# Kernel optimization log

Measured on AMD Instinct MI355X. Metric: run time of the kernel, lower is better.

## Reference

```python
import jax, jax.numpy as jnp
import numpy as np
from jax import lax

B, S, D_MODEL, H, D_CONV, CHUNK = 8, 4096, 1024, 16, 4, 64
D_INNER = D_MODEL


def setup_inputs() -> dict:
    key = jax.random.key(0)
    ks = jax.random.split(key, 6)
    x = jax.random.normal(ks[0], (B, S, D_MODEL), jnp.float32)
    in_proj_w = jax.random.normal(ks[1], (D_INNER + H, D_MODEL), jnp.float32) * 0.02
    conv_w = jax.random.normal(ks[2], (D_INNER, 1, D_CONV), jnp.float32) * 0.3
    conv_b = jnp.zeros((D_INNER,), jnp.float32)
    w_base = jax.random.uniform(ks[3], (H,), jnp.float32, minval=-0.5, maxval=0.5)
    out_proj_w = jax.random.normal(ks[4], (D_MODEL, D_INNER), jnp.float32) * 0.02
    return {"x": x, "in_proj_w": in_proj_w, "conv_w": conv_w, "conv_b": conv_b,
            "w_base": w_base, "out_proj_w": out_proj_w}


def _segsum(a):
    # a: (..., T) -> (..., T, T) with out[i, j] = sum_{k=j+1..i} a[k] for i>=j else -inf
    T = a.shape[-1]
    lower_strict = jnp.tril(jnp.ones((T, T), bool), -1)   # row i > col j
    lower = jnp.tril(jnp.ones((T, T), bool), 0)
    xr = jnp.where(lower_strict, a[..., :, None], 0.0)    # (..., T, T)
    s = jnp.cumsum(xr, axis=-2)
    return jnp.where(lower, s, -jnp.inf)


def _ssd(x, A, l):
    # x: (b, s, h, n); A: (b, s, h); l = chunk size
    b, s, h, n = x.shape
    c = s // l
    x = x.reshape(b, c, l, h, n)
    A = A.reshape(b, c, l, h).transpose(0, 3, 1, 2)        # (b, h, c, l)
    A_cumsum = jnp.cumsum(A, axis=-1)

    # intra-chunk (diagonal) part
    L_log = _segsum(A)                                      # (b, h, c, l, l)
    L = jnp.exp(L_log - jnp.max(L_log, axis=-1, keepdims=True))
    norm_diag = L.sum(-1).transpose(0, 2, 3, 1)             # (b, c, l, h)
    Y_diag = jnp.einsum('bhcls,bcshn->bclhn', L, x)

    # chunk states
    decay_states = A_cumsum[..., -1:] - A_cumsum            # (b, h, c, l)
    decay_states = jnp.exp(decay_states - jnp.max(decay_states, axis=-1, keepdims=True))
    norm_decay = decay_states.sum(-1).transpose(0, 2, 1)    # (b, c, h)
    states = jnp.einsum('bhcl,bclhn->bchn', decay_states, x)

    norm_decay = jnp.pad(norm_decay, ((0, 0), (1, 0), (0, 0)))
    states = jnp.pad(states, ((0, 0), (1, 0), (0, 0), (0, 0)))

    # inter-chunk recurrence
    decay_chunk = _segsum(jnp.pad(A_cumsum[..., -1], ((0, 0), (0, 0), (1, 0))))  # (b,h,c+1,c+1)
    decay_chunk = jnp.exp(decay_chunk - jnp.max(decay_chunk, axis=-1, keepdims=True))
    norm_decay = jnp.einsum('bhzc,bch->bzh', decay_chunk, norm_decay)[:, :-1]    # (b, c, h)
    states = jnp.einsum('bhzc,bchn->bzhn', decay_chunk, states)[:, :-1]          # (b, c, h, n)

    # off-diagonal output
    state_decay_out = jnp.exp(A_cumsum - jnp.max(A_cumsum, axis=-1, keepdims=True))
    norm_off = jnp.einsum('bch,bhcl->bclh', norm_decay, state_decay_out)
    Y_off = jnp.einsum('bchn,bhcl->bclhn', states, state_decay_out)

    Y = (Y_diag + Y_off).reshape(b, s, h, n)
    norm = (norm_diag + norm_off).reshape(b, s, h)
    return Y / norm[..., None]


def reference(x, in_proj_w, conv_w, conv_b, w_base, out_proj_w):
    b, s, d_model = x.shape
    d_inner = in_proj_w.shape[0] - H
    xw = jnp.einsum('bsd,ed->bse', x, in_proj_w)            # (b, s, d_inner + H)
    xi, w = xw[..., :d_inner], xw[..., d_inner:]            # (b,s,d_inner), (b,s,H)
    # causal depthwise conv (padding k-1 on the left == pad both + slice [:s])
    xc = lax.conv_general_dilated(
        xi.transpose(0, 2, 1), conv_w, window_strides=(1,),
        padding=[(D_CONV - 1, 0)], feature_group_count=d_inner,
        dimension_numbers=('NCH', 'OIH', 'NCH'))
    xc = (xc + conv_b[None, :, None]).transpose(0, 2, 1)    # (b, s, d_inner)
    xh = xc.reshape(b, s, H, d_inner // H)                  # (b, s, h, n)
    A = w * w_base                                          # (b, s, H)
    y = _ssd(xh, A, CHUNK)                                  # (b, s, h, n)
    y = y.reshape(b, s, d_inner)
    return jnp.einsum('bsd,ed->bse', y, out_proj_w)         # (b, s, d_model)
```

## Files before the change

### kernel.cpp

```cpp
#include <hip/hip_runtime.h>
#include <hip/hip_bf16.h>
#include <cstdint>

#define B_ 8
#define S_ 4096
#define DM 1024
#define H_ 16
#define DN 64
#define CH 64
#define NC 64
#define M_ (B_ * S_)

typedef unsigned short u16;
typedef u16 u16x8 __attribute__((ext_vector_type(8)));
typedef u16 u16x4 __attribute__((ext_vector_type(4)));
typedef float f32x4 __attribute__((ext_vector_type(4)));
typedef __bf16 bf16x8 __attribute__((ext_vector_type(8)));

__device__ __forceinline__ float bf2f(u16 u) { return __uint_as_float(((unsigned)u) << 16); }
__device__ __forceinline__ u16 f2bf(float f) { __bf16 h = (__bf16)f; return __builtin_bit_cast(u16, h); }

#define GLOAD16(gp, lp) \
  __builtin_amdgcn_global_load_lds((__attribute__((address_space(1))) const void*)(gp), \
                                   (__attribute__((address_space(3))) void*)(lp), 16, 0, 0)
#define BAR()   asm volatile("s_barrier" ::: "memory")
#define VMCNT4() asm volatile("s_waitcnt vmcnt(4)" ::: "memory")
#define VMCNT0() asm volatile("s_waitcnt vmcnt(0)" ::: "memory")

__device__ __forceinline__ void stage_unit(const u16* __restrict__ src, int row0, int kt,
                                           int ks, u16* ldsu, int t, int K) {
#pragma unroll
  for (int i = 0; i < 2; ++i) {
    int f = i * 512 + t;
    int row = f >> 2, j = f & 3;
    int g = j ^ ((row >> 1) & 3);
    GLOAD16(src + (size_t)(row0 + row) * K + kt * 64 + ks * 32 + g * 8, ldsu + f * 8);
  }
}

__device__ __forceinline__ void lda4(bf16x8* fr, const u16* unit, int rbase, int lr, int lk) {
#pragma unroll
  for (int q = 0; q < 4; ++q) {
    int row = rbase + q * 16 + lr;
    int cell = row * 4 + (lk ^ ((row >> 1) & 3));
    fr[q] = *reinterpret_cast<const bf16x8*>(&unit[cell * 8]);
  }
}

__device__ __forceinline__ void mfma16(f32x4 (&acc)[8][4], int mh, const bf16x8* aF, const bf16x8* bF) {
  __builtin_amdgcn_s_setprio(1);
#pragma unroll
  for (int q = 0; q < 4; ++q)
#pragma unroll
    for (int nf = 0; nf < 4; ++nf)
      acc[mh * 4 + q][nf] = __builtin_amdgcn_mfma_f32_16x16x32_bf16(aF[q], bF[nf], acc[mh * 4 + q][nf], 0, 0, 0);
  __builtin_amdgcn_s_setprio(0);
}

template<int MODE>
__global__ __launch_bounds__(512, 2) void bgemm8(
    const u16* __restrict__ A, const u16* __restrict__ Bw,
    void* __restrict__ Cout, int K)
{
  __shared__ u16 lds[8][8192];
  const int orig = blockIdx.x;
  const int swz  = (orig & 7) * 64 + (orig >> 3);
  const int m0 = (swz >> 2) * 256;
  const int n0 = (swz & 3) * 256;
  const int t  = threadIdx.x;
  const int wid = t >> 6, l = t & 63;
  const int wm = wid >> 2, wn = wid & 3;
  const int lr = l & 15, lk = l >> 4;
  const int arb = wm * 128;
  const int brb = wn * 64;

  f32x4 acc[8][4];
#pragma unroll
  for (int i = 0; i < 8; ++i)
#pragma unroll
    for (int j = 0; j < 4; ++j) acc[i][j] = (f32x4){0.f, 0.f, 0.f, 0.f};

  stage_unit(A,  m0, 0, 0, lds[0], t, K);
  stage_unit(Bw, n0, 0, 0, lds[2], t, K);
  stage_unit(A,  m0, 0, 1, lds[1], t, K);
  stage_unit(Bw, n0, 0, 1, lds[3], t, K);
  stage_unit(Bw, n0, 1, 0, lds[6], t, K);
  stage_unit(Bw, n0, 1, 1, lds[7], t, K);
  VMCNT4();
  BAR();

  bf16x8 aF[4], bF0[4], bF1[4];
  for (int i = 0; i < 8; ++i) {
    const bool st = (i < 7);
    lda4(aF, lds[0], arb, lr, lk);
    lda4(bF0, lds[2], brb, lr, lk);
    stage_unit(A, m0, 2 * i + 1, 0, lds[4], t, K);
    BAR(); mfma16(acc, 0, aF, bF0);
    lda4(aF, lds[1], arb, lr, lk);
    lda4(bF1, lds[3], brb, lr, lk);
    stage_unit(A, m0, 2 * i + 1, 1, lds[5], t, K);
    BAR(); mfma16(acc, 0, aF, bF1);
    lda4(aF, lds[0], arb + 64, lr, lk);
    if (st) stage_unit(Bw, n0, 2 * i + 2, 0, lds[2], t, K);
    BAR(); mfma16(acc, 1, aF, bF0);
    lda4(aF, lds[1], arb + 64, lr, lk);
    if (st) stage_unit(Bw, n0, 2 * i + 2, 1, lds[3], t, K);
    if (st) VMCNT4(); else VMCNT0();
    BAR(); mfma16(acc, 1, aF, bF1);
    lda4(aF, lds[4], arb, lr, lk);
    lda4(bF0, lds[6], brb, lr, lk);
    if (st) stage_unit(A, m0, 2 * i + 2, 0, lds[0], t, K);
    BAR(); mfma16(acc, 0, aF, bF0);
    lda4(aF, lds[5], arb, lr, lk);
    lda4(bF1, lds[7], brb, lr, lk);
    if (st) stage_unit(A, m0, 2 * i + 2, 1, lds[1], t, K);
    BAR(); mfma16(acc, 0, aF, bF1);
    lda4(aF, lds[4], arb + 64, lr, lk);
    if (st) stage_unit(Bw, n0, 2 * i + 3, 0, lds[6], t, K);
    BAR(); mfma16(acc, 1, aF, bF0);
    lda4(aF, lds[5], arb + 64, lr, lk);
    if (st) stage_unit(Bw, n0, 2 * i + 3, 1, lds[7], t, K);
    if (st) VMCNT4();
    BAR(); mfma16(acc, 1, aF, bF1);
  }

#pragma unroll
  for (int mf = 0; mf < 8; ++mf) {
#pragma unroll
    for (int nf = 0; nf < 4; ++nf) {
      int n  = n0 + wn * 64 + nf * 16 + lr;
      int mb = m0 + wm * 128 + mf * 16 + lk * 4;
#pragma unroll
      for (int r = 0; r < 4; ++r) {
        if (MODE == 0) ((float*)Cout)[(size_t)(mb + r) * 1024 + n] = acc[mf][nf][r];
        else           ((u16*)Cout)[(size_t)(mb + r) * 1024 + n] = f2bf(acc[mf][nf][r]);
      }
    }
  }
}

__global__ __launch_bounds__(256) void prep_kernel(
    const float* __restrict__ ipw, const float* __restrict__ opw,
    u16* __restrict__ wbf_in, u16* __restrict__ wbf_out, u16* __restrict__ wlo)
{
  int b = blockIdx.x;
  if (b < 1032) {
    const float* src = (b < 520) ? ipw : opw;
    u16* dst = (b < 520) ? wbf_in : wbf_out;
    size_t i = ((size_t)(b < 520 ? b : b - 520) * 256 + threadIdx.x) * 8;
    f32x4 a = *reinterpret_cast<const f32x4*>(&src[i]);
    f32x4 c = *reinterpret_cast<const f32x4*>(&src[i + 4]);
    u16x8 o;
#pragma unroll
    for (int j = 0; j < 4; ++j) { o[j] = f2bf(a[j]); o[4 + j] = f2bf(c[j]); }
    *reinterpret_cast<u16x8*>(&dst[i]) = o;
  } else {
    size_t e = ((size_t)(b - 1032) * 256 + threadIdx.x) * 8;
    f32x4 a = *reinterpret_cast<const f32x4*>(&ipw[1048576 + e]);
    f32x4 c = *reinterpret_cast<const f32x4*>(&ipw[1048576 + e + 4]);
    u16x8 o;
#pragma unroll
    for (int j = 0; j < 4; ++j) {
      u16 h = f2bf(a[j]); o[j]     = f2bf(a[j] - bf2f(h));
      u16 g = f2bf(c[j]); o[4 + j] = f2bf(c[j] - bf2f(g));
    }
    *reinterpret_cast<u16x8*>(&wlo[e]) = o;
  }
}

__global__ __launch_bounds__(256) void wsplit(
    const float* __restrict__ x, const u16* __restrict__ wbf, const u16* __restrict__ wlo,
    u16* __restrict__ xbf, float* __restrict__ wbufT)
{
  __shared__ u16 hi[4][16 * 5 * 8];
  __shared__ u16 lo[4][16 * 5 * 8];
  __shared__ float comb[3][64][4];
  const int t = threadIdx.x;
  const int w = t >> 6, l = t & 63;
  const int r0 = blockIdx.x * 16;
  const int k0 = w * 256;
  const int lr = l & 15, lk = l >> 4;
  const int srow = l >> 2, skc = l & 3;
  u16* HI = hi[w];
  u16* LO = lo[w];

  const float* gx  = &x[(size_t)(r0 + srow) * 1024 + k0 + skc * 8];
  const u16*   gbh = &wbf[(size_t)(1024 + lr) * 1024 + k0 + lk * 8];
  const u16*   gbl = &wlo[(size_t)lr * 1024 + k0 + lk * 8];

  f32x4 a0 = *reinterpret_cast<const f32x4*>(gx);
  f32x4 a1 = *reinterpret_cast<const f32x4*>(gx + 4);
  bf16x8 bh = *reinterpret_cast<const bf16x8*>(gbh);
  bf16x8 bl = *reinterpret_cast<const bf16x8*>(gbl);

  f32x4 acc = (f32x4){0.f, 0.f, 0.f, 0.f};
  const int wcell = srow * 5 + skc;
  const int rcell = lr * 5 + lk;

  for (int kt = 0; kt < 8; ++kt) {
    f32x4 n0, n1; bf16x8 nbh, nbl;
    if (kt < 7) {
      n0  = *reinterpret_cast<const f32x4*>(gx + (kt + 1) * 32);
      n1  = *reinterpret_cast<const f32x4*>(gx + (kt + 1) * 32 + 4);
      nbh = *reinterpret_cast<const bf16x8*>(gbh + (kt + 1) * 32);
      nbl = *reinterpret_cast<const bf16x8*>(gbl + (kt + 1) * 32);
    }
    u16x8 h8, l8;
#pragma unroll
    for (int j = 0; j < 4; ++j) {
      u16 ha = f2bf(a0[j]); h8[j]     = ha; l8[j]     = f2bf(a0[j] - bf2f(ha));
      u16 hb = f2bf(a1[j]); h8[4 + j] = hb; l8[4 + j] = f2bf(a1[j] - bf2f(hb));
    }
    *reinterpret_cast<u16x8*>(&xbf[(size_t)(r0 + srow) * 1024 + k0 + kt * 32 + skc * 8]) = h8;
    *reinterpret_cast<u16x8*>(&HI[wcell * 8]) = h8;
    *reinterpret_cast<u16x8*>(&LO[wcell * 8]) = l8;
    asm volatile("s_waitcnt lgkmcnt(0)" ::: "memory");
    __builtin_amdgcn_sched_barrier(0);
    bf16x8 ah = *reinterpret_cast<const bf16x8*>(&HI[rcell * 8]);
    bf16x8 al = *reinterpret_cast<const bf16x8*>(&LO[rcell * 8]);
    acc = __builtin_amdgcn_mfma_f32_16x16x32_bf16(ah, bh, acc, 0, 0, 0);
    acc = __builtin_amdgcn_mfma_f32_16x16x32_bf16(al, bh, acc, 0, 0, 0);
    acc = __builtin_amdgcn_mfma_f32_16x16x32_bf16(ah, bl, acc, 0, 0, 0);
    a0 = n0; a1 = n1; bh = nbh; bl = nbl;
  }
  if (w) {
#pragma unroll
    for (int r = 0; r < 4; ++r) comb[w - 1][l][r] = acc[r];
  }
  __syncthreads();
  if (!w) {
#pragma unroll
    for (int r = 0; r < 4; ++r) acc[r] += comb[0][l][r] + comb[1][l][r] + comb[2][l][r];
    *reinterpret_cast<f32x4*>(&wbufT[(size_t)lr * M_ + r0 + lk * 4]) = acc;
  }
}

__global__ __launch_bounds__(256) void statesk(
    const u16* __restrict__ xi, const float* __restrict__ cw, const float* __restrict__ cb,
    const float* __restrict__ wbufT, const float* __restrict__ w_base,
    float* __restrict__ Acum, float* __restrict__ acbuf,
    float* __restrict__ states, float* __restrict__ ndbuf)
{
  int bi = blockIdx.x;
  int c  = bi & 63;
  int h  = (bi >> 6) & 15;
  int b  = bi >> 10;
  int bh = b * 16 + h;
  int t  = threadIdx.x;
  __shared__ u16 xis[67][64];
  __shared__ u16 xsT[64][66];
  __shared__ float dsv[CH];
  __shared__ float wls[4][64];
  __shared__ float cbs[64];
  size_t m0 = (size_t)b * S_ + (size_t)c * CH;
  size_t abase = ((size_t)bh * NC + c) * CH;

  wls[t & 3][t >> 2] = cw[(size_t)h * 256 + t];
  if (t < 64) cbs[t] = cb[h * 64 + t];

  {
    int g8  = t & 7;
    int hr0 = t >> 3;
    for (int hr = hr0; hr < 67; hr += 32) {
      u16x8 v = {0, 0, 0, 0, 0, 0, 0, 0};
      if (!(c == 0 && hr < 3))
        v = *reinterpret_cast<const u16x8*>(&xi[(m0 - 3 + hr) * DM + h * 64 + g8 * 8]);
      *reinterpret_cast<u16x8*>(&xis[hr][g8 * 8]) = v;
    }
  }

  if (t < 64) {
    float p = wbufT[(size_t)h * M_ + m0 + t] * w_base[h];
#pragma unroll
    for (int off = 1; off < 64; off <<= 1) {
      float v = __shfl_up(p, off);
      if (t >= off) p += v;
    }
    Acum[abase + t] = p;
    if (t == 63) acbuf[(size_t)bh * NC + c] = p;
    float rmin = p;
#pragma unroll
    for (int off = 1; off < 64; off <<= 1) {
      float v = __shfl_up(rmin, off);
      if (t >= off) rmin = fminf(rmin, v);
    }
    float minall = __shfl(rmin, 63);
    dsv[t] = __expf(minall - p);
  }
  __syncthreads();

  {
    int n  = t & 63;
    int lb = (t >> 6) * 16;
    float w0 = wls[0][n], w1 = wls[1][n], w2 = wls[2][n], w3 = wls[3][n];
    float bias = cbs[n];
    float a = bf2f(xis[lb + 0][n]);
    float bv = bf2f(xis[lb + 1][n]);
    float cv = bf2f(xis[lb + 2][n]);
    u16x8 o0, o1;
#pragma unroll
    for (int r = 0; r < 16; ++r) {
      float dv = bf2f(xis[lb + r + 3][n]);
      float s = fmaf(w3, dv, fmaf(w2, cv, fmaf(w1, bv, fmaf(w0, a, bias))));
      if (r < 8) o0[r] = f2bf(s); else o1[r - 8] = f2bf(s);
      a = bv; bv = cv; cv = dv;
    }
    *reinterpret_cast<u16x8*>(&xsT[n][lb]) = o0;
    *reinterpret_cast<u16x8*>(&xsT[n][lb + 8]) = o1;
  }
  __syncthreads();

  if (t < 64) {
    float acc = 0.f;
#pragma unroll
    for (int l8 = 0; l8 < 64; l8 += 8) {
      u16x8 xv = *reinterpret_cast<const u16x8*>(&xsT[t][l8]);
#pragma unroll
      for (int j = 0; j < 8; ++j) acc = fmaf(dsv[l8 + j], bf2f(xv[j]), acc);
    }
    states[((size_t)bh * NC + c) * DN + t] = acc;
    float v = dsv[t];
#pragma unroll
    for (int off = 32; off >= 1; off >>= 1) v += __shfl_down(v, off);
    if (t == 0) ndbuf[(size_t)bh * NC + c] = v;
  }
}

__global__ __launch_bounds__(256) void interchunk_kernel(
    const float* __restrict__ acbuf, const float* __restrict__ states,
    const float* __restrict__ ndbuf, float* __restrict__ nstates, float* __restrict__ nndbuf)
{
  int bh = blockIdx.x;
  int t  = threadIdx.x;
  __shared__ float Ssum[NC], minP[NC], ndl[NC];
  if (t < 64) {
    float ac = acbuf[(size_t)bh * NC + t];
    float S = ac;
#pragma unroll
    for (int off = 1; off < 64; off <<= 1) {
      float v = __shfl_up(S, off);
      if (t >= off) S += v;
    }
    float Pc = S - ac;
    float mp = Pc;
#pragma unroll
    for (int off = 1; off < 64; off <<= 1) {
      float v = __shfl_up(mp, off);
      if (t >= off) mp = fminf(mp, v);
    }
    Ssum[t] = S;
    minP[t] = mp;
    ndl[t]  = ndbuf[(size_t)bh * NC + t];
  }
  __syncthreads();
  int n  = t & 63;
  int r0 = t >> 6;
  for (int r = 0; r < 16; ++r) {
    int z = r0 + r * 4;
    float mpz = minP[z];
    float acc = 0.f;
    for (int j = 0; j < z; ++j) {
      float e = __expf(mpz - Ssum[j]);
      acc = fmaf(e, states[((size_t)bh * NC + j) * DN + n], acc);
    }
    nstates[((size_t)bh * NC + z) * DN + n] = acc;
  }
  if (t < 64) {
    int z = t;
    float mpz = minP[z];
    float acc = 0.f;
    for (int j = 0; j < z; ++j) acc = fmaf(__expf(mpz - Ssum[j]), ndl[j], acc);
    nndbuf[(size_t)bh * NC + z] = acc;
  }
}

__global__ __launch_bounds__(256) void finalsY(
    const u16* __restrict__ xi, const float* __restrict__ cw, const float* __restrict__ cb,
    const float* __restrict__ Acum, const float* __restrict__ nstates,
    const float* __restrict__ nndbuf, u16* __restrict__ ybuf)
{
  int bi = blockIdx.x;
  int c  = bi & 63;
  int h  = (bi >> 6) & 15;
  int b  = bi >> 10;
  int bh = b * 16 + h;
  int t  = threadIdx.x;
  __shared__ u16 xis[67][64];
  __shared__ u16 xsT[64][66];
  __shared__ float pc[CH], m1s[CH], sdo_s[CH], sto_s[DN], nrm_s[CH];
  __shared__ float wls[4][64];
  __shared__ float cbs[64];
  __shared__ float ndo_s;
  size_t m0 = (size_t)b * S_ + (size_t)c * CH;
  size_t abase = ((size_t)bh * NC + c) * CH;

  wls[t & 3][t >> 2] = cw[(size_t)h * 256 + t];
  if (t < 64) cbs[t] = cb[h * 64 + t];

  {
    int g8  = t & 7;
    int hr0 = t >> 3;
    for (int hr = hr0; hr < 67; hr += 32) {
      u16x8 v = {0, 0, 0, 0, 0, 0, 0, 0};
      if (!(c == 0 && hr < 3))
        v = *reinterpret_cast<const u16x8*>(&xi[(m0 - 3 + hr) * DM + h * 64 + g8 * 8]);
      *reinterpret_cast<u16x8*>(&xis[hr][g8 * 8]) = v;
    }
  }

  if (t < 64) {
    float p = Acum[abase + t];
    pc[t] = p;
    float rmin = p;
#pragma unroll
    for (int off = 1; off < 64; off <<= 1) {
      float v = __shfl_up(rmin, off);
      if (t >= off) rmin = fminf(rmin, v);
    }
    m1s[t] = p - rmin;
    float m3 = p;
#pragma unroll
    for (int off = 32; off >= 1; off >>= 1) m3 = fmaxf(m3, __shfl_down(m3, off));
    m3 = __shfl(m3, 0);
    sdo_s[t] = __expf(p - m3);
    sto_s[t] = nstates[((size_t)bh * NC + c) * DN + t];
    if (t == 0) ndo_s = nndbuf[(size_t)bh * NC + c];
  }
  __syncthreads();

  {
    int n  = t & 63;
    int lb = (t >> 6) * 16;
    float w0 = wls[0][n], w1 = wls[1][n], w2 = wls[2][n], w3 = wls[3][n];
    float bias = cbs[n];
    float a = bf2f(xis[lb + 0][n]);
    float bv = bf2f(xis[lb + 1][n]);
    float cv = bf2f(xis[lb + 2][n]);
    u16x8 o0, o1;
#pragma unroll
    for (int r = 0; r < 16; ++r) {
      float dv = bf2f(xis[lb + r + 3][n]);
      float s = fmaf(w3, dv, fmaf(w2, cv, fmaf(w1, bv, fmaf(w0, a, bias))));
      if (r < 8) o0[r] = f2bf(s); else o1[r - 8] = f2bf(s);
      a = bv; bv = cv; cv = dv;
    }
    *reinterpret_cast<u16x8*>(&xsT[n][lb]) = o0;
    *reinterpret_cast<u16x8*>(&xsT[n][lb + 8]) = o1;
  }
  __syncthreads();

  {
    int w = t >> 6, l = t & 63;
    int lr = l & 15, lk = l >> 4;
    int row = w * 16 + lr;
    float pr = pc[row], m1r = m1s[row];
    bf16x8 afr[2];
    float np = 0.f;
#pragma unroll
    for (int ks = 0; ks < 2; ++ks) {
      int sbase = ks * 32 + lk * 8;
      u16x8 av;
#pragma unroll
      for (int j = 0; j < 8; ++j) {
        int s = sbase + j;
        float L = (s <= row) ? __expf(pr - pc[s] - m1r) : 0.f;
        np += L;
        av[j] = f2bf(L);
      }
      afr[ks] = __builtin_bit_cast(bf16x8, av);
    }
    np += __shfl_xor(np, 16);
    np += __shfl_xor(np, 32);
    if (lk == 0) nrm_s[row] = np;

    f32x4 acc[4];
#pragma unroll
    for (int nf = 0; nf < 4; ++nf) acc[nf] = (f32x4){0.f, 0.f, 0.f, 0.f};
#pragma unroll
    for (int ks = 0; ks < 2; ++ks)
#pragma unroll
      for (int nf = 0; nf < 4; ++nf) {
        bf16x8 bfr = *reinterpret_cast<const bf16x8*>(&xsT[nf * 16 + lr][ks * 32 + lk * 8]);
        acc[nf] = __builtin_amdgcn_mfma_f32_16x16x32_bf16(afr[ks], bfr, acc[nf], 0, 0, 0);
      }
    __syncthreads();
    float ndo = ndo_s;
#pragma unroll
    for (int nf = 0; nf < 4; ++nf)
#pragma unroll
      for (int r = 0; r < 4; ++r) {
        int orow = w * 16 + lk * 4 + r;
        float sd = sdo_s[orow];
        float rec = 1.f / (nrm_s[orow] + ndo * sd);
        float yv = (acc[nf][r] + sto_s[nf * 16 + lr] * sd) * rec;
        ybuf[(m0 + orow) * DM + h * 64 + nf * 16 + lr] = f2bf(yv);
      }
  }
}

extern "C" void kernel_launch(void* const* d_in, const int* in_sizes, int n_in,
                              void* d_out, int out_size, void* d_ws, size_t ws_size,
                              hipStream_t stream) {
  const float* x          = (const float*)d_in[0];
  const float* in_proj_w  = (const float*)d_in[1];
  const float* conv_w     = (const float*)d_in[2];
  const float* conv_b     = (const float*)d_in[3];
  const float* w_base     = (const float*)d_in[4];
  const float* out_proj_w = (const float*)d_in[5];
  float* out = (float*)d_out;
  char* ws = (char*)d_ws;

  u16*   wbf_in  = (u16*)  (ws + 0);
  u16*   wbf_out = (u16*)  (ws + 2129920);
  u16*   wlo16   = (u16*)  (ws + 4227072);
  float* wbufT   = (float*)(ws + 4259840);
  float* Acum    = (float*)(ws + 6356992);
  float* acbuf   = (float*)(ws + 8454144);
  float* states  = (float*)(ws + 10584064);
  float* ndbuf   = (float*)(ws + 12681216);
  float* nstates = (float*)(ws + 12713984);
  float* nndbuf  = (float*)(ws + 14811136);
  u16*   xbf     = (u16*)  (ws + 14843904);
  u16*   xibf    = (u16*)  (ws + 81952768);
  u16*   ybuf    = xbf;

  prep_kernel<<<1040, 256, 0, stream>>>(in_proj_w, out_proj_w, wbf_in, wbf_out, wlo16);
  wsplit<<<2048, 256, 0, stream>>>(x, wbf_in, wlo16, xbf, wbufT);
  bgemm8<1><<<512, 512, 0, stream>>>(xbf, wbf_in, (void*)xibf, DM);
  statesk<<<8192, 256, 0, stream>>>(xibf, conv_w, conv_b, wbufT, w_base,
                                    Acum, acbuf, states, ndbuf);
  interchunk_kernel<<<128, 256, 0, stream>>>(acbuf, states, ndbuf, nstates, nndbuf);
  finalsY<<<8192, 256, 0, stream>>>(xibf, conv_w, conv_b, Acum, nstates, nndbuf, ybuf);
  bgemm8<0><<<512, 512, 0, stream>>>(ybuf, wbf_out, (void*)out, DM);
}
```

Before: 283.4 us.

## Restructure GEMM main loop to four phases of 32 MFMAs per barrier

Reorganizes the bf16 GEMM main loop so each wave loads all eight A fragments and one B fragment set per K-substep and issues 32 MFMAs between barriers, instead of eight phases of 16 MFMAs. A and B staging for the next step are issued together with a tighter prefetch depth, and the prologue no longer preloads the second B K-tile. This halves the number of barriers and LDS reloads of B fragments, at the cost of more live registers for A fragments and less prefetch slack for global loads.

```diff
diff --git a/kernel.cpp b/kernel.cpp
--- a/kernel.cpp
+++ b/kernel.cpp
@@ -47,13 +47,13 @@
   }
 }
 
-__device__ __forceinline__ void mfma16(f32x4 (&acc)[8][4], int mh, const bf16x8* aF, const bf16x8* bF) {
+__device__ __forceinline__ void mfma32(f32x4 (&acc)[8][4], const bf16x8* aF, const bf16x8* bF) {
   __builtin_amdgcn_s_setprio(1);
 #pragma unroll
-  for (int q = 0; q < 4; ++q)
+  for (int q = 0; q < 8; ++q)
 #pragma unroll
     for (int nf = 0; nf < 4; ++nf)
-      acc[mh * 4 + q][nf] = __builtin_amdgcn_mfma_f32_16x16x32_bf16(aF[q], bF[nf], acc[mh * 4 + q][nf], 0, 0, 0);
+      acc[q][nf] = __builtin_amdgcn_mfma_f32_16x16x32_bf16(aF[q], bF[nf], acc[q][nf], 0, 0, 0);
   __builtin_amdgcn_s_setprio(0);
 }
 
@@ -84,44 +84,44 @@
   stage_unit(Bw, n0, 0, 0, lds[2], t, K);
   stage_unit(A,  m0, 0, 1, lds[1], t, K);
   stage_unit(Bw, n0, 0, 1, lds[3], t, K);
-  stage_unit(Bw, n0, 1, 0, lds[6], t, K);
-  stage_unit(Bw, n0, 1, 1, lds[7], t, K);
   VMCNT4();
   BAR();
 
-  bf16x8 aF[4], bF0[4], bF1[4];
+  bf16x8 aF[8], bF[4];
   for (int i = 0; i < 8; ++i) {
     const bool st = (i < 7);
-    lda4(aF, lds[0], arb, lr, lk);
-    lda4(bF0, lds[2], brb, lr, lk);
-    stage_unit(A, m0, 2 * i + 1, 0, lds[4], t, K);
-    BAR(); mfma16(acc, 0, aF, bF0);
-    lda4(aF, lds[1], arb, lr, lk);
-    lda4(bF1, lds[3], brb, lr, lk);
-    stage_unit(A, m0, 2 * i + 1, 1, lds[5], t, K);
-    BAR(); mfma16(acc, 0, aF, bF1);
-    lda4(aF, lds[0], arb + 64, lr, lk);
-    if (st) stage_unit(Bw, n0, 2 * i + 2, 0, lds[2], t, K);
-    BAR(); mfma16(acc, 1, aF, bF0);
-    lda4(aF, lds[1], arb + 64, lr, lk);
-    if (st) stage_unit(Bw, n0, 2 * i + 2, 1, lds[3], t, K);
-    if (st) VMCNT4(); else VMCNT0();
-    BAR(); mfma16(acc, 1, aF, bF1);
-    lda4(aF, lds[4], arb, lr, lk);
-    lda4(bF0, lds[6], brb, lr, lk);
-    if (st) stage_unit(A, m0, 2 * i + 2, 0, lds[0], t, K);
-    BAR(); mfma16(acc, 0, aF, bF0);
-    lda4(aF, lds[5], arb, lr, lk);
-    lda4(bF1, lds[7], brb, lr, lk);
-    if (st) stage_unit(A, m0, 2 * i + 2, 1, lds[1], t, K);
-    BAR(); mfma16(acc, 0, aF, bF1);
-    lda4(aF, lds[4], arb + 64, lr, lk);
-    if (st) stage_unit(Bw, n0, 2 * i + 3, 0, lds[6], t, K);
-    BAR(); mfma16(acc, 1, aF, bF0);
-    lda4(aF, lds[5], arb + 64, lr, lk);
-    if (st) stage_unit(Bw, n0, 2 * i + 3, 1, lds[7], t, K);
-    if (st) VMCNT4();
-    BAR(); mfma16(acc, 1, aF, bF1);
+    lda4(aF,     lds[0], arb,      lr, lk);
+    lda4(aF + 4, lds[0], arb + 64, lr, lk);
+    lda4(bF,     lds[2], brb,      lr, lk);
+    stage_unit(A,  m0, 2 * i + 1, 0, lds[4], t, K);
+    stage_unit(Bw, n0, 2 * i + 1, 0, lds[6], t, K);
+    VMCNT4(); BAR(); mfma32(acc, aF, bF);
+    lda4(aF,     lds[1], arb,      lr, lk);
+    lda4(aF + 4, lds[1], arb + 64, lr, lk);
+    lda4(bF,     lds[3], brb,      lr, lk);
+    stage_unit(A,  m0, 2 * i + 1, 1, lds[5], t, K);
+    stage_unit(Bw, n0, 2 * i + 1, 1, lds[7], t, K);
+    VMCNT4(); BAR(); mfma32(acc, aF, bF);
+    lda4(aF,     lds[4], arb,      lr, lk);
+    lda4(aF + 4, lds[4], arb + 64, lr, lk);
+    lda4(bF,     lds[6], brb,      lr, lk);
+    if (st) {
+      stage_unit(A,  m0, 2 * i + 2, 0, lds[0], t, K);
+      stage_unit(Bw, n0, 2 * i + 2, 0, lds[2], t, K);
+      VMCNT4();
+    } else {
+      VMCNT0();
+    }
+    BAR(); mfma32(acc, aF, bF);
+    lda4(aF,     lds[5], arb,      lr, lk);
+    lda4(aF + 4, lds[5], arb + 64, lr, lk);
+    lda4(bF,     lds[7], brb,      lr, lk);
+    if (st) {
+      stage_unit(A,  m0, 2 * i + 2, 1, lds[1], t, K);
+      stage_unit(Bw, n0, 2 * i + 2, 1, lds[3], t, K);
+      VMCNT4();
+    }
+    BAR(); mfma32(acc, aF, bF);
   }
 
 #pragma unroll
```

Result: no change. 286.5 us (+1.1%).
